# Performance work log

Measured on AMD Instinct MI355X. Metric: run time of the kernel, lower is better.

Reference implementation:

```python
import jax, jax.numpy as jnp
import numpy as np

NUM_CLASSES = 80
IMG = 640
STRIDES = (8, 16, 32)
CENTER_RADIUS = 2.5
TOPK = 10  # n_candidate_k; dynamic_ks = clamp(int(sum top-10 IoU), 1) <= 10


def _make_grids():
    gs, ss = [], []
    for s in STRIDES:
        n = IMG // s
        gy, gx = np.meshgrid(np.arange(n), np.arange(n), indexing="ij")
        gs.append(np.stack([gx.ravel(), gy.ravel()], 1).astype(np.float32))
        ss.append(np.full(n * n, s, np.float32))
    return np.concatenate(gs, 0), np.concatenate(ss, 0)


def setup_inputs() -> dict:
    key = jax.random.key(0)
    B, T, C = 16, 128, NUM_CLASSES
    grid_np, stride_np = _make_grids()
    A = grid_np.shape[0]  # 8400
    k1, k2, k3, k4, k5, k6 = jax.random.split(key, 6)
    # pred boxes: plausible abs xyxy around anchor centers
    ctr = jnp.asarray((grid_np + 0.5) * stride_np[:, None])[None]
    ctr = ctr + 4.0 * jax.random.normal(k1, (B, A, 2))
    wh = jnp.asarray(stride_np)[None, :, None] * jax.random.uniform(k2, (B, A, 2), minval=1.0, maxval=4.0)
    box = jnp.concatenate([ctr - wh / 2, ctr + wh / 2], -1)
    logits = 2.0 * jax.random.normal(k3, (B, A, 1 + C))
    pred = jnp.concatenate([box, logits], -1)  # [B, A, 5+C]
    # targets: [B, T, 6] = (batch_id, cid, x1, y1, x2, y2)
    tc = jax.random.uniform(k4, (B, T, 2), minval=60.0, maxval=580.0)
    twh = jax.random.uniform(k5, (B, T, 2), minval=30.0, maxval=200.0)
    tbox = jnp.concatenate([tc - twh / 2, tc + twh / 2], -1)
    cid = jax.random.randint(k6, (B, T, 1), 0, C).astype(jnp.float32)
    bid = jnp.broadcast_to(jnp.arange(B, dtype=jnp.float32)[:, None, None], (B, T, 1))
    target = jnp.concatenate([bid, cid, tbox], -1)
    return {"pred": pred, "target": target,
            "grid_mask": jnp.asarray(grid_np), "stride_mask": jnp.asarray(stride_np)}


def _pairwise_iou(a, b):
    # a [T,4], b [A,4], xyxy -> [T,A]
    lt = jnp.maximum(a[:, None, :2], b[None, :, :2])
    rb = jnp.minimum(a[:, None, 2:], b[None, :, 2:])
    wh = jnp.clip(rb - lt, 0.0, None)
    inter = wh[..., 0] * wh[..., 1]
    area_a = jnp.clip(a[:, 2] - a[:, 0], 0.0, None) * jnp.clip(a[:, 3] - a[:, 1], 0.0, None)
    area_b = jnp.clip(b[:, 2] - b[:, 0], 0.0, None) * jnp.clip(b[:, 3] - b[:, 1], 0.0, None)
    return inter / (area_a[:, None] + area_b[None, :] - inter + 1e-8)


def _ciou(p, t):
    # complete IoU, elementwise over leading dims, xyxy
    lt = jnp.maximum(p[..., :2], t[..., :2])
    rb = jnp.minimum(p[..., 2:], t[..., 2:])
    wh = jnp.clip(rb - lt, 0.0, None)
    inter = wh[..., 0] * wh[..., 1]
    wp, hp = p[..., 2] - p[..., 0], p[..., 3] - p[..., 1]
    wt, ht = t[..., 2] - t[..., 0], t[..., 3] - t[..., 1]
    iou = inter / (wp * hp + wt * ht - inter + 1e-8)
    cwh = jnp.maximum(p[..., 2:], t[..., 2:]) - jnp.minimum(p[..., :2], t[..., :2])
    c2 = cwh[..., 0] ** 2 + cwh[..., 1] ** 2 + 1e-8
    rho2 = (((p[..., 0] + p[..., 2]) - (t[..., 0] + t[..., 2])) ** 2
            + ((p[..., 1] + p[..., 3]) - (t[..., 1] + t[..., 3])) ** 2) / 4.0
    v = (4.0 / jnp.pi ** 2) * (jnp.arctan(wt / (ht + 1e-8)) - jnp.arctan(wp / (hp + 1e-8))) ** 2
    alpha = v / (1.0 - iou + v + 1e-8)
    return iou - rho2 / c2 - alpha * v


def _bce_logits(x, t):
    return jnp.maximum(x, 0.0) - x * t + jnp.log1p(jnp.exp(-jnp.abs(x)))


def _assign_image(pred_i, tgt_i, grid, stride):
    # pred_i [A,5+C], tgt_i [T,6]
    A, T, C = pred_i.shape[0], tgt_i.shape[0], NUM_CLASSES
    tbox = tgt_i[:, 2:6]
    cid = tgt_i[:, 1].astype(jnp.int32)
    xc = (grid[:, 0] + 0.5) * stride  # [A]
    yc = (grid[:, 1] + 0.5) * stride
    d = jnp.stack([xc[None] - tbox[:, 0:1], yc[None] - tbox[:, 1:2],
                   tbox[:, 2:3] - xc[None], tbox[:, 3:4] - yc[None]], -1)  # [T,A,4]
    in_boxes = d.min(-1) > 0.0  # [T,A]
    txc = (tbox[:, 0] + tbox[:, 2]) / 2
    tyc = (tbox[:, 1] + tbox[:, 3]) / 2
    in_centers = jnp.maximum(jnp.abs(xc[None] - txc[:, None]),
                             jnp.abs(yc[None] - tyc[:, None])) < CENTER_RADIUS * stride[None]
    in_box = in_boxes.any(0) | in_centers.any(0)  # [A], candidate anchors
    in_box_center = in_boxes & in_centers  # [T,A]
    iou = jnp.where(in_box[None], _pairwise_iou(tbox, pred_i[:, :4]), 0.0)  # [T,A]
    iou_cost = -jnp.log(iou + 1e-8)
    prob = jnp.sqrt(jax.nn.sigmoid(pred_i[:, 4:5]) * jax.nn.sigmoid(pred_i[:, 5:]))  # [A,C]
    logp = jnp.maximum(jnp.log(prob), -100.0)      # torch BCE clamps log at -100
    log1mp = jnp.maximum(jnp.log1p(-prob), -100.0)
    # sum_c BCE(prob, onehot(cid)) computed analytically (avoids [T,A,C]):
    cls_cost = -(log1mp.sum(-1)[None, :] + (logp - log1mp)[:, cid].T)  # [T,A]
    # 1e9 keeps anchors outside in_box out of the candidate pool (original slices them away)
    cost = cls_cost + 3.0 * iou_cost + 1e5 * (~in_box_center) + 1e9 * (~in_box)[None, :]
    topk_ious, _ = jax.lax.top_k(iou, TOPK)  # [T,10]
    dyn_k = jnp.maximum(topk_ious.sum(1).astype(jnp.int32), 1)  # [T]
    _, idx = jax.lax.top_k(-cost, TOPK)  # 10 lowest-cost anchors per target
    sel = jnp.arange(TOPK)[None, :] < dyn_k[:, None]  # keep first dyn_k of them
    matching = jnp.zeros((T, A), bool).at[jnp.arange(T)[:, None], idx].set(sel)
    matching = matching & in_box[None, :]
    conflict = matching.sum(0) > 1  # anchors claimed by >1 targets
    keep = jnp.arange(T)[:, None] == jnp.argmin(cost, 0)[None, :]  # [T,A]
    matching = jnp.where(conflict[None, :], keep, matching)
    mp = matching.any(0)  # [A]
    tp = jnp.argmax(matching, 0)  # [A] target index per anchor
    p_iou = jnp.clip((iou / (iou.max(1, keepdims=True) + 1e-8)).max(0), 0.0, 1.0)  # [A]
    obj_t = jnp.where(in_box, p_iou, 0.0)
    box_t = tbox[tp]  # [A,4]
    cls_t = jax.nn.one_hot(cid[tp], C, dtype=jnp.float32)  # [A,C]
    return mp, box_t, obj_t, cls_t


def reference(pred, target, grid_mask, stride_mask):
    B, A = pred.shape[:2]
    C = NUM_CLASSES
    mp, box_t, obj_t, cls_t = jax.lax.stop_gradient(
        jax.vmap(_assign_image, in_axes=(0, 0, None, None))(pred, target, grid_mask, stride_mask))
    m = mp.reshape(-1).astype(pred.dtype)  # matched-anchor mask over B*A
    n = jnp.maximum(m.sum(), 1.0)
    p = pred.reshape(B * A, -1)
    lbox = 0.05 * jnp.sum((1.0 - _ciou(p[:, :4], box_t.reshape(-1, 4))) * m) / n
    lobj = _bce_logits(p[:, 4], obj_t.reshape(-1)).mean()
    lcls = 0.5 * jnp.sum(_bce_logits(p[:, 5:], cls_t.reshape(-1, C)).mean(-1) * m) / n
    loss = lbox + lobj + lcls
    return loss, jnp.stack([lbox, lobj, lcls])
```

## Files before the change

kernel.cpp:

```cpp
#include <hip/hip_runtime.h>
#include <cfloat>

#pragma clang fp contract(off)

#define NCLS 80
#define PDIM 85
#define NA   8400
#define NB   16
#define NT   128
#define NTOP 10
#define APB  64
#define BPI  132
#define LN2  0.6931471805599453f
#define CAPW 512

#define KSENT 0xFFFFFFFF7FFFFFFFull

__device__ __forceinline__ float sigm_fast(float x){
  float e = __expf(-x);
  return __builtin_amdgcn_rcpf(1.0f + e);
}

__device__ __forceinline__ float bce_fast(float x, float t){
  float ax = fabsf(x);
  float e  = __expf(-ax);
  return fmaxf(x,0.0f) - x*t + LN2*__builtin_amdgcn_logf(1.0f + e);
}

__device__ __forceinline__ float pair_iou(float tx1,float ty1,float tx2,float ty2,
                                          float px1,float py1,float px2,float py2){
  float w = fminf(tx2,px2) - fmaxf(tx1,px1);
  float h = fminf(ty2,py2) - fmaxf(ty1,py1);
  w = fmaxf(w,0.0f); h = fmaxf(h,0.0f);
  float inter = w*h;
  float at = fmaxf(tx2-tx1,0.0f)*fmaxf(ty2-ty1,0.0f);
  float ap = fmaxf(px2-px1,0.0f)*fmaxf(py2-py1,0.0f);
  float den = at+ap-inter+1e-8f;
  return inter * __builtin_amdgcn_rcpf(den);
}

__device__ __forceinline__ float dval_fn(float sobj, float lg){
  float ln_sobj = LN2*__builtin_amdgcn_logf(sobj);
  float e = __expf(-fabsf(lg));
  float L = LN2*__builtin_amdgcn_logf(1.0f + e);
  float ln_sc = -(fmaxf(-lg,0.0f) + L);
  float lph = 0.5f*(ln_sobj + ln_sc);
  float p = __expf(lph);
  float lp = fmaxf(lph, -100.0f);
  float l1 = fmaxf(LN2*__builtin_amdgcn_logf(fmaxf(1.0f - p, 0.0f)), -100.0f);
  return lp - l1;
}

__device__ __forceinline__ float cost_from(float S, float dval, float iou, bool ibc, bool ib){
  float iouc = -LN2 * __builtin_amdgcn_logf(iou + 1e-8f);
  float clsc = -(S + dval);
  float c = clsc + 3.0f*iouc;
  c = c + (ibc ? 0.0f : 100000.0f);
  c = c + (ib  ? 0.0f : 1000000000.0f);
  return c;
}

__device__ __forceinline__ unsigned long long key_of(float c, int idx){
  unsigned int u = __float_as_uint(c);
  u ^= (u & 0x80000000u) ? 0xFFFFFFFFu : 0x80000000u;
  return ((unsigned long long)u << 32) | (unsigned int)idx;
}

__device__ __forceinline__ void ins_iou(float* riou, float iou){
  if (iou > riou[NTOP-1]){
    #pragma unroll
    for (int j = NTOP-1; j >= 1; --j){
      bool gj  = iou > riou[j];
      bool gj1 = iou > riou[j-1];
      riou[j] = gj ? (gj1 ? riou[j-1] : iou) : riou[j];
    }
    riou[0] = (iou > riou[0]) ? iou : riou[0];
  }
}
__device__ __forceinline__ void ins_key(unsigned long long* rk, unsigned long long key){
  if (key < rk[NTOP-1]){
    #pragma unroll
    for (int j = NTOP-1; j >= 1; --j){
      bool bj  = key < rk[j];
      bool bj1 = key < rk[j-1];
      rk[j] = bj ? (bj1 ? rk[j-1] : key) : rk[j];
    }
    rk[0] = (key < rk[0]) ? key : rk[0];
  }
}

__global__ __launch_bounds__(256) void k0_precompute(
    const float* __restrict__ pred, const float* __restrict__ target,
    const float* __restrict__ grid, const float* __restrict__ stridev,
    float4* __restrict__ pbox4, float4* __restrict__ meta4,
    float* __restrict__ obja, float* __restrict__ sobja,
    float* __restrict__ S0a, float* __restrict__ D, int use_d,
    unsigned long long* __restrict__ mask, float* __restrict__ acc)
{
  __shared__ float  tile[APB*PDIM];
  __shared__ float4 tb4s[NT];
  __shared__ float  ps_s[4][APB];
  __shared__ float  ps0_s[4][APB];
  __shared__ int    ib_s[4][APB];

  int i  = blockIdx.x / BPI;
  int b  = blockIdx.x % BPI;
  int c0 = b*APB;
  int n  = NA - c0; if (n > APB) n = APB;
  int tid = threadIdx.x;

  if (blockIdx.x == 0) acc[tid] = 0.0f;

  const float* src = pred + ((size_t)i*NA + c0)*PDIM;
  int tot = n*PDIM;
  for (int idx = tid; idx < tot; idx += 256) tile[idx] = src[idx];
  for (int idx = tid; idx < NT; idx += 256){
    const float* tg = target + (i*NT + idx)*6;
    tb4s[idx] = make_float4(tg[2],tg[3],tg[4],tg[5]);
  }
  __syncthreads();

  int al = tid & 63, cg = tid >> 6;
  if (al < n){
    int gid = i*NA + c0 + al;
    float x4 = tile[al*PDIM+4];
    float e4 = __expf(-fabsf(x4));
    float L4 = LN2*__builtin_amdgcn_logf(1.0f + e4);
    float ln_sobj = -(fmaxf(-x4,0.0f) + L4);
    float ps = 0.0f, ps0 = 0.0f;
    #pragma unroll 4
    for (int k = 0; k < 20; ++k){
      int c = cg*20 + k;
      float x  = tile[al*PDIM+5+c];
      float e  = __expf(-fabsf(x));
      float L  = LN2*__builtin_amdgcn_logf(1.0f + e);
      float ln_sc = -(fmaxf(-x,0.0f) + L);
      float lph = 0.5f*(ln_sobj + ln_sc);
      float p   = __expf(lph);
      float lp  = fmaxf(lph, -100.0f);
      float l1  = fmaxf(LN2*__builtin_amdgcn_logf(fmaxf(1.0f - p, 0.0f)), -100.0f);
      ps  += l1;
      if (use_d) D[(size_t)c*((size_t)NB*NA) + gid] = lp - l1;
      ps0 += fmaxf(x,0.0f) + L;
    }
    ps_s[cg][al] = ps; ps0_s[cg][al] = ps0;

    int ga = c0 + al;
    float xg = grid[2*ga], yg = grid[2*ga+1], sv = stridev[ga];
    float xc = (xg + 0.5f)*sv, yc = (yg + 0.5f)*sv;
    float rc = 2.5f*sv;
    bool ibp = false;
    #pragma unroll 4
    for (int t = cg*32; t < cg*32+32; ++t){
      float4 T = tb4s[t];
      bool inb = (xc-T.x>0.0f)&&(yc-T.y>0.0f)&&(T.z-xc>0.0f)&&(T.w-yc>0.0f);
      float txc=(T.x+T.z)*0.5f, tyc=(T.y+T.w)*0.5f;
      bool inc = fmaxf(fabsf(xc-txc),fabsf(yc-tyc)) < rc;
      ibp = ibp || inb || inc;
    }
    ib_s[cg][al] = ibp ? 1 : 0;
  }
  __syncthreads();

  if (tid < n){
    int a = tid;
    int gid = i*NA + c0 + a;
    float s  = ps_s[0][a]  + ps_s[1][a]  + ps_s[2][a]  + ps_s[3][a];
    float s0 = ps0_s[0][a] + ps0_s[1][a] + ps0_s[2][a] + ps0_s[3][a];
    bool ib  = (ib_s[0][a] | ib_s[1][a] | ib_s[2][a] | ib_s[3][a]) != 0;

    float x1 = tile[a*PDIM+0], y1 = tile[a*PDIM+1];
    float x2 = tile[a*PDIM+2], y2 = tile[a*PDIM+3];
    float ol = tile[a*PDIM+4];
    pbox4[gid] = make_float4(x1,y1,x2,y2);
    obja[gid]  = ol;
    sobja[gid] = sigm_fast(ol);
    S0a[gid]   = s0;
    mask[(size_t)gid*2]   = 0ull;
    mask[(size_t)gid*2+1] = 0ull;

    int ga = c0 + a;
    float xg = grid[2*ga], yg = grid[2*ga+1], sv = stridev[ga];
    float xc = (xg + 0.5f)*sv, yc = (yg + 0.5f)*sv;
    float rc = 2.5f*sv;
    meta4[gid] = make_float4(xc, yc, ib ? rc : -rc, s);
  }
}

__global__ __launch_bounds__(256) void k1_pertarget(
    const float4* __restrict__ pbox4, const float4* __restrict__ meta4,
    const float* __restrict__ D, int use_d,
    const float* __restrict__ sobja, const float* __restrict__ pred,
    const float* __restrict__ target,
    float* __restrict__ rowmax, unsigned long long* __restrict__ mask)
{
  __shared__ __align__(16) int2 seg[4*CAPW];
  __shared__ int   cnts_s[4], cibc_s[4];
  __shared__ float wiou[4][NTOP];
  __shared__ unsigned long long wkey[4][NTOP];

  int tid = threadIdx.x, lane = tid & 63, w = tid >> 6;
  int g = blockIdx.x;
  int i = g / NT, t = g - i*NT;
  int iNA = i*NA;
  const size_t BA = (size_t)NB*NA;
  const float* m4f = (const float*)meta4;

  const float* tg = target + (size_t)g*6;
  int   cid = (int)tg[1];
  float tx1 = tg[2], ty1 = tg[3], tx2 = tg[4], ty2 = tg[5];
  float txc = (tx1+tx2)*0.5f, tyc = (ty1+ty2)*0.5f;
  const float* Dc = use_d ? (D + (size_t)cid*BA) : nullptr;

  int cnt = 0, ci = 0;
  int a = w*64 + lane;
  float4 pb = pbox4[iNA+a];
  float4 mt = meta4[iNA+a];
  for (int k = 0; k < 33; ++k){
    int a2 = a + 256;
    int ld = (a2 < NA) ? a2 : a;
    float4 pbn = pbox4[iNA+ld];
    float4 mtn = meta4[iNA+ld];

    bool act = (a < NA) && (mt.z > 0.0f);
    float iou = 0.0f; bool ibc = false;
    if (act){
      iou = pair_iou(tx1,ty1,tx2,ty2, pb.x,pb.y,pb.z,pb.w);
      bool inb = (mt.x-tx1>0.0f)&&(mt.y-ty1>0.0f)&&(tx2-mt.x>0.0f)&&(ty2-mt.y>0.0f);
      bool inc = fmaxf(fabsf(mt.x-txc),fabsf(mt.y-tyc)) < mt.z;
      ibc = inb && inc;
    }
    bool cand = (iou > 0.0f) || ibc;
    unsigned long long bb  = __ballot(cand);
    unsigned long long bb2 = __ballot(ibc);
    if (cand){
      int pos = cnt + __popcll(bb & ((1ull << lane) - 1ull));
      if (pos < CAPW) seg[w*CAPW + pos] = make_int2(a | (ibc ? (1<<15) : 0), __float_as_int(iou));
    }
    cnt += __popcll(bb);
    ci  += __popcll(bb2);
    pb = pbn; mt = mtn; a = a2;
  }
  if (lane == 0){ cnts_s[w] = cnt; cibc_s[w] = ci; }
  __syncthreads();

  int tibc = cibc_s[0]+cibc_s[1]+cibc_s[2]+cibc_s[3];
  bool ovf = (cnts_s[0]>CAPW)||(cnts_s[1]>CAPW)||(cnts_s[2]>CAPW)||(cnts_s[3]>CAPW);
  bool fastp = !ovf && (tibc >= 16);

  float riou[NTOP]; unsigned long long rk[NTOP];
  #pragma unroll
  for (int j=0;j<NTOP;++j){ riou[j]=0.0f; rk[j]=KSENT; }

  if (fastp){
    int cw = cnts_s[w];
    for (int j = lane; j < cw; j += 64){
      int2 e = seg[w*CAPW + j];
      int a1 = e.x & 0x7fff;
      bool ibc = (e.x >> 15) != 0;
      float iou = __int_as_float(e.y);
      ins_iou(riou, iou);
      int gid = iNA + a1;
      float S  = m4f[(size_t)gid*4 + 3];
      float dv = use_d ? Dc[gid] : dval_fn(sobja[gid], pred[(size_t)gid*PDIM + 5 + cid]);
      float c  = cost_from(S, dv, iou, ibc, true);
      ins_key(rk, key_of(c, a1));
    }
  } else {
    for (int a1 = tid; a1 < NA; a1 += 256){
      float4 mt2 = meta4[iNA+a1];
      if (mt2.z > 0.0f){
        float4 pb2 = pbox4[iNA+a1];
        float iou = pair_iou(tx1,ty1,tx2,ty2, pb2.x,pb2.y,pb2.z,pb2.w);
        ins_iou(riou, iou);
        bool inb = (mt2.x-tx1>0.0f)&&(mt2.y-ty1>0.0f)&&(tx2-mt2.x>0.0f)&&(ty2-mt2.y>0.0f);
        bool inc = fmaxf(fabsf(mt2.x-txc),fabsf(mt2.y-tyc)) < mt2.z;
        float dv = use_d ? Dc[iNA+a1] : dval_fn(sobja[iNA+a1], pred[(size_t)(iNA+a1)*PDIM + 5 + cid]);
        float c = cost_from(mt2.w, dv, iou, inb&&inc, true);
        ins_key(rk, key_of(c, a1));
      }
    }
  }

  #pragma unroll
  for (int r = 0; r < NTOP; ++r){
    float gm = riou[0];
    #pragma unroll
    for (int m = 1; m < 64; m <<= 1) gm = fmaxf(gm, __shfl_xor(gm, m));
    unsigned long long bb = __ballot(riou[0] == gm);
    int win = __ffsll(bb) - 1;
    if (lane == win){
      #pragma unroll
      for (int j=0;j<NTOP-1;++j) riou[j] = riou[j+1];
      riou[NTOP-1] = 0.0f;
    }
    if (lane == 0) wiou[w][r] = gm;
  }
  #pragma unroll
  for (int r = 0; r < NTOP; ++r){
    unsigned long long gk = rk[0];
    #pragma unroll
    for (int m = 1; m < 64; m <<= 1){
      unsigned long long o = __shfl_xor(gk, m);
      gk = (o < gk) ? o : gk;
    }
    unsigned long long bb = __ballot(rk[0] == gk);
    int win = __ffsll(bb) - 1;
    if (lane == win){
      #pragma unroll
      for (int j=0;j<NTOP-1;++j) rk[j] = rk[j+1];
      rk[NTOP-1] = KSENT;
    }
    if (lane == 0) wkey[w][r] = gk;
  }
  __syncthreads();

  if (w == 0){
    int p0=0,p1=0,p2=0,p3=0;
    float ssum = 0.0f, rmax = 0.0f;
    #pragma unroll
    for (int r = 0; r < NTOP; ++r){
      float v0=wiou[0][p0], v1=wiou[1][p1], v2=wiou[2][p2], v3=wiou[3][p3];
      float mx = fmaxf(fmaxf(v0,v1), fmaxf(v2,v3));
      if (r == 0) rmax = mx;
      ssum += mx;
      if      (mx == v0) ++p0;
      else if (mx == v1) ++p1;
      else if (mx == v2) ++p2;
      else               ++p3;
    }
    int dk = (int)ssum;
    if (dk < 1) dk = 1;

    int q0=0,q1=0,q2=0,q3=0;
    int myidx = 0x7fffffff;
    #pragma unroll
    for (int r = 0; r < NTOP; ++r){
      unsigned long long k0=wkey[0][q0], k1=wkey[1][q1], k2=wkey[2][q2], k3=wkey[3][q3];
      unsigned long long mn = k0;
      mn = (k1 < mn) ? k1 : mn;
      mn = (k2 < mn) ? k2 : mn;
      mn = (k3 < mn) ? k3 : mn;
      if (lane == r) myidx = (int)(mn & 0xFFFFFFFFull);
      if      (mn == k0) ++q0;
      else if (mn == k1) ++q1;
      else if (mn == k2) ++q2;
      else               ++q3;
    }

    if (lane == 0) rowmax[g] = rmax;
    if (lane < NTOP && lane < dk){
      int a1 = myidx;
      if (a1 >= 0 && a1 < NA){
        atomicOr(&mask[(size_t)(iNA + a1)*2 + (t>>6)], 1ull << (t & 63));
      }
    }
  }
}

__global__ __launch_bounds__(256) void k2_peranchor(
    const float* __restrict__ pred,
    const float4* __restrict__ pbox4, const float4* __restrict__ meta4,
    const float* __restrict__ obja, const float* __restrict__ sobja,
    const float* __restrict__ S0a,
    const float* __restrict__ D, int use_d,
    const float* __restrict__ target,
    const float* __restrict__ rowmax, const unsigned long long* __restrict__ mask,
    float* __restrict__ acc)
{
  __shared__ float4 tb4[NT];
  __shared__ int    tcid[NT];
  __shared__ float  invm[NT];
  __shared__ float  tarea[NT];
  __shared__ float  sh_obj[4][64];
  __shared__ float  sh_c[4][64];
  __shared__ int    sh_tp[4][64];

  int i  = blockIdx.x / BPI;
  int b  = blockIdx.x % BPI;
  int c0 = b*APB;
  int q  = threadIdx.x & 63;
  int s  = threadIdx.x >> 6;
  int a  = c0 + q;
  const size_t BA = (size_t)NB*NA;

  for (int idx = threadIdx.x; idx < NT; idx += 256){
    const float* tg = target + (i*NT + idx)*6;
    tcid[idx] = (int)tg[1];
    float x1=tg[2], y1=tg[3], x2=tg[4], y2=tg[5];
    tb4[idx]   = make_float4(x1,y1,x2,y2);
    invm[idx]  = 1.0f / (rowmax[i*NT + idx] + 1e-8f);
    tarea[idx] = fmaxf(x2-x1,0.0f)*fmaxf(y2-y1,0.0f);
  }
  __syncthreads();

  bool valid = (a < NA);
  int gid = i*NA + a;
  float4 pb = valid ? pbox4[gid] : make_float4(0,0,0,0);
  float4 mt = valid ? meta4[gid] : make_float4(0,0,-1.0f,0);
  bool ib = valid && (mt.z > 0.0f);
  float rc = fabsf(mt.z);
  float px1=pb.x, py1=pb.y, px2=pb.z, py2=pb.w;
  float ap = fmaxf(px2-px1,0.0f)*fmaxf(py2-py1,0.0f);

  float best = 0.0f;
  if (ib){
    #pragma unroll 4
    for (int t = s*32; t < s*32+32; ++t){
      float4 T = tb4[t];
      float w = fminf(T.z,px2) - fmaxf(T.x,px1);
      float h = fminf(T.w,py2) - fmaxf(T.y,py1);
      w = fmaxf(w,0.0f); h = fmaxf(h,0.0f);
      float inter = w*h;
      float den = tarea[t] + ap - inter + 1e-8f;
      float iou = inter * __builtin_amdgcn_rcpf(den);
      best = fmaxf(best, iou*invm[t]);
    }
  }
  sh_obj[s][q] = best;

  unsigned long long m0=0, m1=0;
  if (valid){ m0 = mask[(size_t)gid*2]; m1 = mask[(size_t)gid*2+1]; }
  int cnt = __popcll(m0) + __popcll(m1);

  float bc = FLT_MAX; int bt = NT;
  if (cnt > 1){
    float sobj = use_d ? 0.0f : sobja[gid];
    float Sg = mt.w;
    for (int t = s*32; t < s*32+32; ++t){
      float4 T = tb4[t];
      float iou = ib ? pair_iou(T.x,T.y,T.z,T.w,px1,py1,px2,py2) : 0.0f;
      bool inb = (mt.x-T.x>0.0f)&&(mt.y-T.y>0.0f)&&(T.z-mt.x>0.0f)&&(T.w-mt.y>0.0f);
      float txc=(T.x+T.z)*0.5f, tyc=(T.y+T.w)*0.5f;
      bool inc = fmaxf(fabsf(mt.x-txc),fabsf(mt.y-tyc)) < rc;
      float dv = use_d ? D[(size_t)tcid[t]*BA + gid]
                       : dval_fn(sobj, pred[(size_t)gid*PDIM + 5 + tcid[t]]);
      float c = cost_from(Sg, dv, iou, inb&&inc, ib);
      if (c < bc){ bc = c; bt = t; }
    }
  }
  sh_c[s][q] = bc; sh_tp[s][q] = bt;
  __syncthreads();

  if (s == 0){
    float m=0.0f, vbox=0.0f, vobj=0.0f, vcls=0.0f;
    if (valid){
      float ob = fmaxf(fmaxf(sh_obj[0][q],sh_obj[1][q]), fmaxf(sh_obj[2][q],sh_obj[3][q]));
      float obj_t = ib ? fminf(fmaxf(ob,0.0f),1.0f) : 0.0f;
      vobj = bce_fast(obja[gid], obj_t);

      float cbest = sh_c[0][q]; int tbest = sh_tp[0][q];
      #pragma unroll
      for (int s2=1; s2<4; ++s2){
        float cs = sh_c[s2][q]; int ts = sh_tp[s2][q];
        if (cs < cbest){ cbest = cs; tbest = ts; }
      }

      int tp = 0; bool mpv = false;
      if (cnt > 1){ tp = tbest; mpv = true; }
      else if (cnt == 1){
        tp = m0 ? (__ffsll(m0)-1) : (64 + __ffsll(m1)-1);
        mpv = true;
      }

      if (mpv){
        m = 1.0f;
        float4 T = tb4[tp];
        float x1=T.x, y1=T.y, x2=T.z, y2=T.w;
        float w = fmaxf(fminf(px2,x2)-fmaxf(px1,x1),0.0f);
        float h = fmaxf(fminf(py2,y2)-fmaxf(py1,y1),0.0f);
        float inter = w*h;
        float wp=px2-px1, hp=py2-py1, wt=x2-x1, ht=y2-y1;
        float iou = inter/(wp*hp + wt*ht - inter + 1e-8f);
        float cw = fmaxf(px2,x2)-fminf(px1,x1);
        float ch = fmaxf(py2,y2)-fminf(py1,y1);
        float c2 = cw*cw + ch*ch + 1e-8f;
        float dx = (px1+px2)-(x1+x2), dy = (py1+py2)-(y1+y2);
        float rho2 = (dx*dx + dy*dy)/4.0f;
        float da = atanf(wt/(ht+1e-8f)) - atanf(wp/(hp+1e-8f));
        float v  = 0.4052847345693511f * da * da;
        float alpha = v/(1.0f - iou + v + 1e-8f);
        vbox = 1.0f - (iou - rho2/c2 - alpha*v);

        int cc = tcid[tp];
        float xcc = pred[(size_t)gid*PDIM + 5 + cc];
        vcls = (S0a[gid] - xcc) * (1.0f/80.0f);
      }
    }

    #pragma unroll
    for (int off=32; off>0; off>>=1){
      m    += __shfl_down(m, off);
      vbox += __shfl_down(vbox, off);
      vobj += __shfl_down(vobj, off);
      vcls += __shfl_down(vcls, off);
    }
    if (q == 0){
      int slot = (blockIdx.x & 63)*4;
      atomicAdd(&acc[slot+0], m);
      atomicAdd(&acc[slot+1], vbox);
      atomicAdd(&acc[slot+2], vobj);
      atomicAdd(&acc[slot+3], vcls);
    }
  }
}

__global__ void k3_final(const float* __restrict__ acc, float* __restrict__ out){
  int l = threadIdx.x;
  float4 v = ((const float4*)acc)[l];
  #pragma unroll
  for (int off=32; off>0; off>>=1){
    v.x += __shfl_down(v.x, off);
    v.y += __shfl_down(v.y, off);
    v.z += __shfl_down(v.z, off);
    v.w += __shfl_down(v.w, off);
  }
  if (l == 0){
    float n    = fmaxf(v.x, 1.0f);
    float lbox = 0.05f * v.y / n;
    float lobj = v.z / (float)(NB*NA);
    float lcls = 0.5f  * v.w / n;
    out[0] = lbox + lobj + lcls;
    out[1] = lbox; out[2] = lobj; out[3] = lcls;
  }
}

extern "C" void kernel_launch(void* const* d_in, const int* in_sizes, int n_in,
                              void* d_out, int out_size, void* d_ws, size_t ws_size,
                              hipStream_t stream) {
  const float* pred    = (const float*)d_in[0];
  const float* target  = (const float*)d_in[1];
  const float* grid    = (const float*)d_in[2];
  const float* stridev = (const float*)d_in[3];
  float* out = (float*)d_out;

  char* ws = (char*)d_ws;
  const size_t BA = (size_t)NB*NA;

  size_t off = 0;
  unsigned long long* mask = (unsigned long long*)(ws + off); off += BA*16;
  float* acc    = (float*)(ws + off); off += 64*4*4;
  float4* pbox4 = (float4*)(ws + off); off += BA*16;
  float4* meta4 = (float4*)(ws + off); off += BA*16;
  float* obja   = (float*)(ws + off); off += BA*4;
  float* sobja  = (float*)(ws + off); off += BA*4;
  float* S0a    = (float*)(ws + off); off += BA*4;
  float* rowmax = (float*)(ws + off); off += (size_t)NB*NT*4;
  float* D      = (float*)(ws + off);
  const size_t need_d = off + (size_t)NCLS*BA*4;
  int use_d = (ws_size >= need_d) ? 1 : 0;

  k0_precompute<<<NB*BPI, 256, 0, stream>>>(pred, target, grid, stridev,
                                            pbox4, meta4, obja, sobja, S0a, D, use_d,
                                            mask, acc);
  k1_pertarget <<<NB*NT,  256, 0, stream>>>(pbox4, meta4, D, use_d,
                                            sobja, pred, target, rowmax, mask);
  k2_peranchor <<<NB*BPI, 256, 0, stream>>>(pred, pbox4, meta4, obja, sobja, S0a,
                                            D, use_d, target, rowmax, mask, acc);
  k3_final     <<<1, 64, 0, stream>>>(acc, out);
}
```

Before: 183.2 us.

## Pad anchor arrays, defer IoU to candidate pass, fold final reduce into k2

```diff
diff --git a/kernel.cpp b/kernel.cpp
--- a/kernel.cpp
+++ b/kernel.cpp
@@ -6,13 +6,16 @@
 #define NCLS 80
 #define PDIM 85
 #define NA   8400
+#define NAP  8448
 #define NB   16
 #define NT   128
 #define NTOP 10
 #define APB  64
 #define BPI  132
 #define LN2  0.6931471805599453f
-#define CAPW 512
+#define CAPW 768
+
+#define BAPC ((size_t)NB*NAP)
 
 #define KSENT 0xFFFFFFFF7FFFFFFFull
 
@@ -95,7 +98,8 @@
     float4* __restrict__ pbox4, float4* __restrict__ meta4,
     float* __restrict__ obja, float* __restrict__ sobja,
     float* __restrict__ S0a, float* __restrict__ D, int use_d,
-    unsigned long long* __restrict__ mask, float* __restrict__ acc)
+    unsigned long long* __restrict__ mask, float* __restrict__ acc,
+    unsigned int* __restrict__ done)
 {
   __shared__ float  tile[APB*PDIM];
   __shared__ float4 tb4s[NT];
@@ -109,7 +113,10 @@
   int n  = NA - c0; if (n > APB) n = APB;
   int tid = threadIdx.x;
 
-  if (blockIdx.x == 0) acc[tid] = 0.0f;
+  if (blockIdx.x == 0){
+    acc[tid] = 0.0f;
+    if (tid == 0) *done = 0u;
+  }
 
   const float* src = pred + ((size_t)i*NA + c0)*PDIM;
   int tot = n*PDIM;
@@ -122,7 +129,7 @@
 
   int al = tid & 63, cg = tid >> 6;
   if (al < n){
-    int gid = i*NA + c0 + al;
+    int gid = i*NAP + c0 + al;
     float x4 = tile[al*PDIM+4];
     float e4 = __expf(-fabsf(x4));
     float L4 = LN2*__builtin_amdgcn_logf(1.0f + e4);
@@ -140,7 +147,7 @@
       float lp  = fmaxf(lph, -100.0f);
       float l1  = fmaxf(LN2*__builtin_amdgcn_logf(fmaxf(1.0f - p, 0.0f)), -100.0f);
       ps  += l1;
-      if (use_d) D[(size_t)c*((size_t)NB*NA) + gid] = lp - l1;
+      if (use_d) D[(size_t)c*BAPC + gid] = lp - l1;
       ps0 += fmaxf(x,0.0f) + L;
     }
     ps_s[cg][al] = ps; ps0_s[cg][al] = ps0;
@@ -164,7 +171,7 @@
 
   if (tid < n){
     int a = tid;
-    int gid = i*NA + c0 + a;
+    int gid = i*NAP + c0 + a;
     float s  = ps_s[0][a]  + ps_s[1][a]  + ps_s[2][a]  + ps_s[3][a];
     float s0 = ps0_s[0][a] + ps0_s[1][a] + ps0_s[2][a] + ps0_s[3][a];
     bool ib  = (ib_s[0][a] | ib_s[1][a] | ib_s[2][a] | ib_s[3][a]) != 0;
@@ -184,6 +191,10 @@
     float xc = (xg + 0.5f)*sv, yc = (yg + 0.5f)*sv;
     float rc = 2.5f*sv;
     meta4[gid] = make_float4(xc, yc, ib ? rc : -rc, s);
+  } else if (tid < APB){
+    int gid = i*NAP + c0 + tid;
+    meta4[gid] = make_float4(0.0f, 0.0f, -1.0f, 0.0f);
+    pbox4[gid] = make_float4(0.0f, 0.0f, 0.0f, 0.0f);
   }
 }
 
@@ -194,7 +205,7 @@
     const float* __restrict__ target,
     float* __restrict__ rowmax, unsigned long long* __restrict__ mask)
 {
-  __shared__ __align__(16) int2 seg[4*CAPW];
+  __shared__ int   seg[4*CAPW];
   __shared__ int   cnts_s[4], cibc_s[4];
   __shared__ float wiou[4][NTOP];
   __shared__ unsigned long long wkey[4][NTOP];
@@ -202,40 +213,38 @@
   int tid = threadIdx.x, lane = tid & 63, w = tid >> 6;
   int g = blockIdx.x;
   int i = g / NT, t = g - i*NT;
-  int iNA = i*NA;
-  const size_t BA = (size_t)NB*NA;
+  int iNAP = i*NAP;
+  int iNA  = i*NA;
   const float* m4f = (const float*)meta4;
 
   const float* tg = target + (size_t)g*6;
   int   cid = (int)tg[1];
   float tx1 = tg[2], ty1 = tg[3], tx2 = tg[4], ty2 = tg[5];
   float txc = (tx1+tx2)*0.5f, tyc = (ty1+ty2)*0.5f;
-  const float* Dc = use_d ? (D + (size_t)cid*BA) : nullptr;
+  const float* Dc = use_d ? (D + (size_t)cid*BAPC) : nullptr;
 
   int cnt = 0, ci = 0;
   int a = w*64 + lane;
-  float4 pb = pbox4[iNA+a];
-  float4 mt = meta4[iNA+a];
+  float4 pb = pbox4[iNAP+a];
+  float4 mt = meta4[iNAP+a];
   for (int k = 0; k < 33; ++k){
     int a2 = a + 256;
-    int ld = (a2 < NA) ? a2 : a;
-    float4 pbn = pbox4[iNA+ld];
-    float4 mtn = meta4[iNA+ld];
-
-    bool act = (a < NA) && (mt.z > 0.0f);
-    float iou = 0.0f; bool ibc = false;
-    if (act){
-      iou = pair_iou(tx1,ty1,tx2,ty2, pb.x,pb.y,pb.z,pb.w);
-      bool inb = (mt.x-tx1>0.0f)&&(mt.y-ty1>0.0f)&&(tx2-mt.x>0.0f)&&(ty2-mt.y>0.0f);
-      bool inc = fmaxf(fabsf(mt.x-txc),fabsf(mt.y-tyc)) < mt.z;
-      ibc = inb && inc;
-    }
-    bool cand = (iou > 0.0f) || ibc;
+    int ld = (a2 < NAP) ? a2 : 0;
+    float4 pbn = pbox4[iNAP+ld];
+    float4 mtn = meta4[iNAP+ld];
+
+    bool act = (mt.z > 0.0f);
+    bool ov  = (fminf(tx2,pb.z) > fmaxf(tx1,pb.x)) &&
+               (fminf(ty2,pb.w) > fmaxf(ty1,pb.y));
+    bool inb = (mt.x-tx1>0.0f)&&(mt.y-ty1>0.0f)&&(tx2-mt.x>0.0f)&&(ty2-mt.y>0.0f);
+    bool inc = fmaxf(fabsf(mt.x-txc),fabsf(mt.y-tyc)) < mt.z;
+    bool ibc = inb && inc;
+    bool cand = act && (ov || ibc);
     unsigned long long bb  = __ballot(cand);
     unsigned long long bb2 = __ballot(ibc);
     if (cand){
       int pos = cnt + __popcll(bb & ((1ull << lane) - 1ull));
-      if (pos < CAPW) seg[w*CAPW + pos] = make_int2(a | (ibc ? (1<<15) : 0), __float_as_int(iou));
+      if (pos < CAPW) seg[w*CAPW + pos] = a | (ibc ? (1<<15) : 0);
     }
     cnt += __popcll(bb);
     ci  += __popcll(bb2);
@@ -255,27 +264,28 @@
   if (fastp){
     int cw = cnts_s[w];
     for (int j = lane; j < cw; j += 64){
-      int2 e = seg[w*CAPW + j];
-      int a1 = e.x & 0x7fff;
-      bool ibc = (e.x >> 15) != 0;
-      float iou = __int_as_float(e.y);
+      int e  = seg[w*CAPW + j];
+      int a1 = e & 0x3fff;
+      bool ibc = (e & (1<<15)) != 0;
+      int gid = iNAP + a1;
+      float4 pb2 = pbox4[gid];
+      float iou = pair_iou(tx1,ty1,tx2,ty2, pb2.x,pb2.y,pb2.z,pb2.w);
       ins_iou(riou, iou);
-      int gid = iNA + a1;
       float S  = m4f[(size_t)gid*4 + 3];
-      float dv = use_d ? Dc[gid] : dval_fn(sobja[gid], pred[(size_t)gid*PDIM + 5 + cid]);
+      float dv = use_d ? Dc[gid] : dval_fn(sobja[gid], pred[(size_t)(iNA+a1)*PDIM + 5 + cid]);
       float c  = cost_from(S, dv, iou, ibc, true);
       ins_key(rk, key_of(c, a1));
     }
   } else {
     for (int a1 = tid; a1 < NA; a1 += 256){
-      float4 mt2 = meta4[iNA+a1];
+      float4 mt2 = meta4[iNAP+a1];
       if (mt2.z > 0.0f){
-        float4 pb2 = pbox4[iNA+a1];
+        float4 pb2 = pbox4[iNAP+a1];
         float iou = pair_iou(tx1,ty1,tx2,ty2, pb2.x,pb2.y,pb2.z,pb2.w);
         ins_iou(riou, iou);
         bool inb = (mt2.x-tx1>0.0f)&&(mt2.y-ty1>0.0f)&&(tx2-mt2.x>0.0f)&&(ty2-mt2.y>0.0f);
         bool inc = fmaxf(fabsf(mt2.x-txc),fabsf(mt2.y-tyc)) < mt2.z;
-        float dv = use_d ? Dc[iNA+a1] : dval_fn(sobja[iNA+a1], pred[(size_t)(iNA+a1)*PDIM + 5 + cid]);
+        float dv = use_d ? Dc[iNAP+a1] : dval_fn(sobja[iNAP+a1], pred[(size_t)(iNA+a1)*PDIM + 5 + cid]);
         float c = cost_from(mt2.w, dv, iou, inb&&inc, true);
         ins_key(rk, key_of(c, a1));
       }
@@ -352,7 +362,7 @@
     if (lane < NTOP && lane < dk){
       int a1 = myidx;
       if (a1 >= 0 && a1 < NA){
-        atomicOr(&mask[(size_t)(iNA + a1)*2 + (t>>6)], 1ull << (t & 63));
+        atomicOr(&mask[(size_t)(iNAP + a1)*2 + (t>>6)], 1ull << (t & 63));
       }
     }
   }
@@ -366,7 +376,8 @@
     const float* __restrict__ D, int use_d,
     const float* __restrict__ target,
     const float* __restrict__ rowmax, const unsigned long long* __restrict__ mask,
-    float* __restrict__ acc)
+    float* __restrict__ acc, float* __restrict__ out,
+    unsigned int* __restrict__ done)
 {
   __shared__ float4 tb4[NT];
   __shared__ int    tcid[NT];
@@ -382,7 +393,6 @@
   int q  = threadIdx.x & 63;
   int s  = threadIdx.x >> 6;
   int a  = c0 + q;
-  const size_t BA = (size_t)NB*NA;
 
   for (int idx = threadIdx.x; idx < NT; idx += 256){
     const float* tg = target + (i*NT + idx)*6;
@@ -395,7 +405,8 @@
   __syncthreads();
 
   bool valid = (a < NA);
-  int gid = i*NA + a;
+  int gid = i*NAP + a;
+  size_t pbase = (size_t)(i*NA + a)*PDIM;
   float4 pb = valid ? pbox4[gid] : make_float4(0,0,0,0);
   float4 mt = valid ? meta4[gid] : make_float4(0,0,-1.0f,0);
   bool ib = valid && (mt.z > 0.0f);
@@ -433,8 +444,8 @@
       bool inb = (mt.x-T.x>0.0f)&&(mt.y-T.y>0.0f)&&(T.z-mt.x>0.0f)&&(T.w-mt.y>0.0f);
       float txc=(T.x+T.z)*0.5f, tyc=(T.y+T.w)*0.5f;
       bool inc = fmaxf(fabsf(mt.x-txc),fabsf(mt.y-tyc)) < rc;
-      float dv = use_d ? D[(size_t)tcid[t]*BA + gid]
-                       : dval_fn(sobj, pred[(size_t)gid*PDIM + 5 + tcid[t]]);
+      float dv = use_d ? D[(size_t)tcid[t]*BAPC + gid]
+                       : dval_fn(sobj, pred[pbase + 5 + tcid[t]]);
       float c = cost_from(Sg, dv, iou, inb&&inc, ib);
       if (c < bc){ bc = c; bt = t; }
     }
@@ -483,7 +494,7 @@
         vbox = 1.0f - (iou - rho2/c2 - alpha*v);
 
         int cc = tcid[tp];
-        float xcc = pred[(size_t)gid*PDIM + 5 + cc];
+        float xcc = pred[pbase + 5 + cc];
         vcls = (S0a[gid] - xcc) * (1.0f/80.0f);
       }
     }
@@ -495,33 +506,41 @@
       vobj += __shfl_down(vobj, off);
       vcls += __shfl_down(vcls, off);
     }
+
+    unsigned int fin = 0;
     if (q == 0){
       int slot = (blockIdx.x & 63)*4;
       atomicAdd(&acc[slot+0], m);
       atomicAdd(&acc[slot+1], vbox);
       atomicAdd(&acc[slot+2], vobj);
       atomicAdd(&acc[slot+3], vcls);
-    }
-  }
-}
-
-__global__ void k3_final(const float* __restrict__ acc, float* __restrict__ out){
-  int l = threadIdx.x;
-  float4 v = ((const float4*)acc)[l];
-  #pragma unroll
-  for (int off=32; off>0; off>>=1){
-    v.x += __shfl_down(v.x, off);
-    v.y += __shfl_down(v.y, off);
-    v.z += __shfl_down(v.z, off);
-    v.w += __shfl_down(v.w, off);
-  }
-  if (l == 0){
-    float n    = fmaxf(v.x, 1.0f);
-    float lbox = 0.05f * v.y / n;
-    float lobj = v.z / (float)(NB*NA);
-    float lcls = 0.5f  * v.w / n;
-    out[0] = lbox + lobj + lcls;
-    out[1] = lbox; out[2] = lobj; out[3] = lcls;
+      __threadfence();
+      fin = atomicAdd(done, 1u) + 1u;
+    }
+    fin = __shfl(fin, 0);
+    if (fin == gridDim.x){
+      __threadfence();
+      float4 v;
+      v.x = atomicAdd(&acc[q*4+0], 0.0f);
+      v.y = atomicAdd(&acc[q*4+1], 0.0f);
+      v.z = atomicAdd(&acc[q*4+2], 0.0f);
+      v.w = atomicAdd(&acc[q*4+3], 0.0f);
+      #pragma unroll
+      for (int off=32; off>0; off>>=1){
+        v.x += __shfl_down(v.x, off);
+        v.y += __shfl_down(v.y, off);
+        v.z += __shfl_down(v.z, off);
+        v.w += __shfl_down(v.w, off);
+      }
+      if (q == 0){
+        float n    = fmaxf(v.x, 1.0f);
+        float lbox = 0.05f * v.y / n;
+        float lobj = v.z / (float)(NB*NA);
+        float lcls = 0.5f  * v.w / n;
+        out[0] = lbox + lobj + lcls;
+        out[1] = lbox; out[2] = lobj; out[3] = lcls;
+      }
+    }
   }
 }
 
@@ -535,27 +554,27 @@
   float* out = (float*)d_out;
 
   char* ws = (char*)d_ws;
-  const size_t BA = (size_t)NB*NA;
 
   size_t off = 0;
-  unsigned long long* mask = (unsigned long long*)(ws + off); off += BA*16;
+  unsigned long long* mask = (unsigned long long*)(ws + off); off += BAPC*16;
   float* acc    = (float*)(ws + off); off += 64*4*4;
-  float4* pbox4 = (float4*)(ws + off); off += BA*16;
-  float4* meta4 = (float4*)(ws + off); off += BA*16;
-  float* obja   = (float*)(ws + off); off += BA*4;
-  float* sobja  = (float*)(ws + off); off += BA*4;
-  float* S0a    = (float*)(ws + off); off += BA*4;
+  unsigned int* done = (unsigned int*)(ws + off); off += 16;
+  float4* pbox4 = (float4*)(ws + off); off += BAPC*16;
+  float4* meta4 = (float4*)(ws + off); off += BAPC*16;
+  float* obja   = (float*)(ws + off); off += BAPC*4;
+  float* sobja  = (float*)(ws + off); off += BAPC*4;
+  float* S0a    = (float*)(ws + off); off += BAPC*4;
   float* rowmax = (float*)(ws + off); off += (size_t)NB*NT*4;
   float* D      = (float*)(ws + off);
-  const size_t need_d = off + (size_t)NCLS*BA*4;
+  const size_t need_d = off + (size_t)NCLS*BAPC*4;
   int use_d = (ws_size >= need_d) ? 1 : 0;
 
   k0_precompute<<<NB*BPI, 256, 0, stream>>>(pred, target, grid, stridev,
                                             pbox4, meta4, obja, sobja, S0a, D, use_d,
-                                            mask, acc);
+                                            mask, acc, done);
   k1_pertarget <<<NB*NT,  256, 0, stream>>>(pbox4, meta4, D, use_d,
                                             sobja, pred, target, rowmax, mask);
   k2_peranchor <<<NB*BPI, 256, 0, stream>>>(pred, pbox4, meta4, obja, sobja, S0a,
-                                            D, use_d, target, rowmax, mask, acc);
-  k3_final     <<<1, 64, 0, stream>>>(acc, out);
-}
+                                            D, use_d, target, rowmax, mask, acc,
+                                            out, done);
+}
```

Measured after the change: 209.9 us. 1.15x slower.
